# Kernel optimization log

Hardware: AMD Instinct MI355X
Metric: run time of the kernel (lower is better)

Reference implementation:

```python
import jax, jax.numpy as jnp
import numpy as np

B, S, D, H = 4, 1024, 1024, 16
DEPTH = D // H


def setup_inputs() -> dict:
    key = jax.random.key(0)
    ks = jax.random.split(key, 12)
    scale = 1.0 / np.sqrt(D)
    return {
        "query": jax.random.normal(ks[0], (B, S, D), jnp.float32),
        "key_in": jax.random.normal(ks[1], (B, S, D), jnp.float32),
        "value": jax.random.normal(ks[2], (B, S, D), jnp.float32),
        "mask": jnp.zeros((B, 1, 1, S), jnp.float32),
        "wq": jax.random.normal(ks[3], (D, D), jnp.float32) * scale,
        "bq": jnp.zeros((D,), jnp.float32),
        "wk": jax.random.normal(ks[4], (D, D), jnp.float32) * scale,
        "bk": jnp.zeros((D,), jnp.float32),
        "wv": jax.random.normal(ks[5], (D, D), jnp.float32) * scale,
        "bv": jnp.zeros((D,), jnp.float32),
        "wo": jax.random.normal(ks[6], (D, D), jnp.float32) * scale,
        "bo": jnp.zeros((D,), jnp.float32),
    }


def _split_heads(x):
    b, s, _ = x.shape
    return x.reshape(b, s, H, DEPTH).transpose(0, 2, 1, 3)  # [B,H,S,depth]


def reference(query, key_in, value, mask, wq, bq, wk, bk, wv, bv, wo, bo):
    q = _split_heads(query @ wq + bq)
    k = _split_heads(key_in @ wk + bk)
    v = _split_heads(value @ wv + bv)
    # scaled dot-product attention, full O(S^2) scores as in the original
    scores = jnp.einsum("bhqd,bhkd->bhqk", q, k) / jnp.sqrt(jnp.float32(DEPTH))
    scores = scores + mask * (-1e9)
    attn = jax.nn.softmax(scores, axis=-1)
    ctx = jnp.einsum("bhqk,bhkd->bhqd", attn, v)
    concat = ctx.transpose(0, 2, 1, 3).reshape(query.shape[0], -1, D)
    return concat @ wo + bo
```

## Files before the change

kernel.cpp:

```cpp
#include <hip/hip_runtime.h>
#include <hip/hip_bf16.h>
#include <stdint.h>

#define B_ 4
#define S_ 1024
#define D_ 1024
#define H_ 16
#define DEPTH_ 64

typedef __attribute__((ext_vector_type(8))) short bf16x8;
typedef __attribute__((ext_vector_type(4))) float f32x4;
typedef unsigned short ubf16;

#define BAR() do { asm volatile("" ::: "memory"); __builtin_amdgcn_s_barrier(); asm volatile("" ::: "memory"); } while (0)

__device__ __forceinline__ ubf16 f2bf(float f) {
  union { float f; unsigned u; } v; v.f = f;
  unsigned r = v.u + 0x7fffu + ((v.u >> 16) & 1u);
  return (ubf16)(r >> 16);
}

__device__ __forceinline__ void async16(void* lds, const void* g) {
  __builtin_amdgcn_global_load_lds(
      (const __attribute__((address_space(1))) void*)g,
      (__attribute__((address_space(3))) void*)lds, 16, 0, 0);
}

struct Tp4 { const float* W[4]; ubf16* WT[4]; };
__global__ __launch_bounds__(256) void transpose4_bf16(Tp4 a) {
  __shared__ float tile[32][33];
  const float* W = a.W[blockIdx.z];
  ubf16* WT = a.WT[blockIdx.z];
  int n0 = blockIdx.x * 32, k0 = blockIdx.y * 32;
  int tx = threadIdx.x & 31, ty = threadIdx.x >> 5;
#pragma unroll
  for (int i = 0; i < 4; ++i)
    tile[ty + i * 8][tx] = W[(size_t)(k0 + ty + i * 8) * D_ + n0 + tx];
  __syncthreads();
#pragma unroll
  for (int i = 0; i < 4; ++i)
    WT[(size_t)(n0 + ty + i * 8) * D_ + k0 + tx] = f2bf(tile[tx][ty + i * 8]);
}

struct GemmUnitF {
  const float* A; const ubf16* BT; const float* bias; void* out; int mode;
};
struct GemmArgsF { GemmUnitF u[3]; };

__global__ __launch_bounds__(512) void gemm_qkv_fused(GemmArgsF args) {
  const int lin = blockIdx.x;
  const int wg = (lin & 7) * 48 + (lin >> 3);
  const int z = wg >> 7, rr = wg & 127;
  const GemmUnitF gu = args.u[z];
  const int bm0 = (rr >> 2) * 128;
  const int bn0 = (rr & 3) * 256;
  const int tid = threadIdx.x, wid = tid >> 6, lane = tid & 63;
  const int wm = wid >> 2, wn = wid & 3;
  const int l15 = lane & 15, l4 = lane >> 4;
  const int K = 1024;

  __shared__ __align__(16) ubf16 As[2][128 * 32];
  __shared__ __align__(16) ubf16 Bs[2][256 * 32];
  f32x4 acc[4][4] = {};

  const float* aP0;
  {
    int r0 = tid >> 2, s0 = tid & 3, g0 = s0 ^ ((r0 >> 1) & 3);
    aP0 = gu.A + (size_t)(bm0 + r0) * K + g0 * 8;
  }
  const ubf16* bP0; const ubf16* bP1;
  {
    int c0 = tid;        int r0 = c0 >> 2, s0 = c0 & 3, g0 = s0 ^ ((r0 >> 1) & 3);
    int c1 = 512 + tid;  int r1 = c1 >> 2, s1 = c1 & 3, g1 = s1 ^ ((r1 >> 1) & 3);
    bP0 = gu.BT + (size_t)(bn0 + r0) * K + g0 * 8;
    bP1 = gu.BT + (size_t)(bn0 + r1) * K + g1 * 8;
  }
  int aOff[4], bOff[4];
#pragma unroll
  for (int f = 0; f < 4; ++f) {
    int ra = wm * 64 + f * 16 + l15;
    aOff[f] = ra * 64 + (l4 ^ ((ra >> 1) & 3)) * 16;
    int rb = wn * 64 + f * 16 + l15;
    bOff[f] = rb * 64 + (l4 ^ ((rb >> 1) & 3)) * 16;
  }

  {
    f32x4 a00 = *(const f32x4*)aP0, a01 = *(const f32x4*)(aP0 + 4); aP0 += 32;
    async16((char*)&Bs[0][0] + wid * 1024, bP0); bP0 += 32;
    async16((char*)&Bs[0][0] + 8192 + wid * 1024, bP1); bP1 += 32;
    bf16x8 w0;
#pragma unroll
    for (int q = 0; q < 4; ++q) {
      w0[q] = (short)f2bf(a00[q]); w0[4 + q] = (short)f2bf(a01[q]);
    }
    *(bf16x8*)((char*)&As[0][0] + tid * 16) = w0;
    asm volatile("s_waitcnt lgkmcnt(0)" ::: "memory");
  }

#pragma unroll 1
  for (int t = 0; t < 31; ++t) {
    const int cur = t & 1;
    f32x4 a00 = *(const f32x4*)aP0, a01 = *(const f32x4*)(aP0 + 4); aP0 += 32;
    async16((char*)&Bs[cur ^ 1][0] + wid * 1024, bP0); bP0 += 32;
    async16((char*)&Bs[cur ^ 1][0] + 8192 + wid * 1024, bP1); bP1 += 32;
    __builtin_amdgcn_sched_barrier(0);
    asm volatile("s_waitcnt vmcnt(4)" ::: "memory");
    __builtin_amdgcn_s_barrier();
    __builtin_amdgcn_sched_barrier(0);
    bf16x8 af[4], bfr[4];
#pragma unroll
    for (int mi = 0; mi < 4; ++mi)
      af[mi] = *(const bf16x8*)((const char*)&As[cur][0] + aOff[mi]);
#pragma unroll
    for (int ni = 0; ni < 4; ++ni)
      bfr[ni] = *(const bf16x8*)((const char*)&Bs[cur][0] + bOff[ni]);
#pragma unroll
    for (int mi = 0; mi < 4; ++mi)
#pragma unroll
      for (int ni = 0; ni < 4; ++ni)
        acc[mi][ni] = __builtin_amdgcn_mfma_f32_16x16x32_bf16(af[mi], bfr[ni], acc[mi][ni], 0, 0, 0);
    __builtin_amdgcn_sched_barrier(0);
    bf16x8 w0;
#pragma unroll
    for (int q = 0; q < 4; ++q) {
      w0[q] = (short)f2bf(a00[q]); w0[4 + q] = (short)f2bf(a01[q]);
    }
    *(bf16x8*)((char*)&As[cur ^ 1][0] + tid * 16) = w0;
    asm volatile("s_waitcnt lgkmcnt(0)" ::: "memory");
    __builtin_amdgcn_s_barrier();
  }
  asm volatile("s_waitcnt vmcnt(0)" ::: "memory");
  __builtin_amdgcn_s_barrier();
  {
    bf16x8 af[4], bfr[4];
#pragma unroll
    for (int mi = 0; mi < 4; ++mi)
      af[mi] = *(const bf16x8*)((const char*)&As[1][0] + aOff[mi]);
#pragma unroll
    for (int ni = 0; ni < 4; ++ni)
      bfr[ni] = *(const bf16x8*)((const char*)&Bs[1][0] + bOff[ni]);
#pragma unroll
    for (int mi = 0; mi < 4; ++mi)
#pragma unroll
      for (int ni = 0; ni < 4; ++ni)
        acc[mi][ni] = __builtin_amdgcn_mfma_f32_16x16x32_bf16(af[mi], bfr[ni], acc[mi][ni], 0, 0, 0);
  }

  float bv[4];
#pragma unroll
  for (int ni = 0; ni < 4; ++ni) bv[ni] = gu.bias[bn0 + wn * 64 + ni * 16 + l15];
#pragma unroll
  for (int mi = 0; mi < 4; ++mi) {
#pragma unroll
    for (int ni = 0; ni < 4; ++ni) {
#pragma unroll
      for (int r = 0; r < 4; ++r) {
        int m = bm0 + wm * 64 + mi * 16 + l4 * 4 + r;
        int n = bn0 + wn * 64 + ni * 16 + l15;
        float v = acc[mi][ni][r] + bv[ni];
        if (gu.mode == 0) {
          ((ubf16*)gu.out)[(size_t)m * 1024 + n] = f2bf(v);
        } else {
          int b = m >> 10, s = m & 1023, h = n >> 6, d = n & 63;
          ((ubf16*)gu.out)[(((size_t)(b * H_ + h)) * DEPTH_ + d) * S_ + s] = f2bf(v);
        }
      }
    }
  }
}

struct GemmUnit {
  const ubf16* A; const ubf16* BT; const float* bias; void* out; int mode;
};
struct GemmArgs { GemmUnit u[3]; };

__global__ __launch_bounds__(256) void gemm_bt(GemmArgs args, int M, int N) {
  const GemmUnit gu = args.u[blockIdx.z];
  const int orig = blockIdx.x + (blockIdx.y << 3);
  const int xcd = orig & 7, j = orig >> 3;
  const int bm0 = (xcd * 4 + (j & 3)) * 128;
  const int bn0 = (j >> 2) * 128;
  const int tid = threadIdx.x, wid = tid >> 6, lane = tid & 63;
  const int wr = wid >> 1, wc = wid & 1;
  const int l15 = lane & 15, l4 = lane >> 4;
  const int K = 1024;

  __shared__ __align__(16) ubf16 As[2][128 * 32];
  __shared__ __align__(16) ubf16 Bs[2][128 * 32];
  f32x4 acc[4][4] = {};

  const ubf16* aCur[2]; const ubf16* bCur[2];
#pragma unroll
  for (int i = 0; i < 2; ++i) {
    int c = i * 256 + tid;
    int r = c >> 2, s = c & 3;
    int cg = s ^ ((r >> 1) & 3);
    aCur[i] = gu.A + (size_t)(bm0 + r) * K + cg * 8;
    bCur[i] = gu.BT + (size_t)(bn0 + r) * K + cg * 8;
  }
  auto stageAdv = [&](int bf) {
#pragma unroll
    for (int i = 0; i < 2; ++i) {
      async16((char*)&As[bf][0] + i * 4096 + wid * 1024, aCur[i]);
      async16((char*)&Bs[bf][0] + i * 4096 + wid * 1024, bCur[i]);
      aCur[i] += 32; bCur[i] += 32;
    }
  };
  int aOff[4], bOff[4];
#pragma unroll
  for (int f = 0; f < 4; ++f) {
    int ra = wr * 64 + f * 16 + l15;
    aOff[f] = ra * 64 + (l4 ^ ((ra >> 1) & 3)) * 16;
    int rb = wc * 64 + f * 16 + l15;
    bOff[f] = rb * 64 + (l4 ^ ((rb >> 1) & 3)) * 16;
  }

  stageAdv(0);
  for (int t = 0; t < 32; ++t) {
    const int cur = t & 1;
    if (t < 31) {
      stageAdv(cur ^ 1);
      asm volatile("s_waitcnt vmcnt(4)" ::: "memory");
    } else {
      asm volatile("s_waitcnt vmcnt(0)" ::: "memory");
    }
    BAR();
    bf16x8 af[4], bfr[4];
#pragma unroll
    for (int mi = 0; mi < 4; ++mi)
      af[mi] = *(const bf16x8*)((const char*)&As[cur][0] + aOff[mi]);
#pragma unroll
    for (int ni = 0; ni < 4; ++ni)
      bfr[ni] = *(const bf16x8*)((const char*)&Bs[cur][0] + bOff[ni]);
#pragma unroll
    for (int mi = 0; mi < 4; ++mi)
#pragma unroll
      for (int ni = 0; ni < 4; ++ni)
        acc[mi][ni] = __builtin_amdgcn_mfma_f32_16x16x32_bf16(af[mi], bfr[ni], acc[mi][ni], 0, 0, 0);
    BAR();
  }

  float bv[4];
#pragma unroll
  for (int ni = 0; ni < 4; ++ni) bv[ni] = gu.bias[bn0 + wc * 64 + ni * 16 + l15];
#pragma unroll
  for (int mi = 0; mi < 4; ++mi) {
#pragma unroll
    for (int ni = 0; ni < 4; ++ni) {
#pragma unroll
      for (int r = 0; r < 4; ++r) {
        int m = bm0 + wr * 64 + mi * 16 + l4 * 4 + r;
        int n = bn0 + wc * 64 + ni * 16 + l15;
        float v = acc[mi][ni][r] + bv[ni];
        if (gu.mode == 0) {
          ((ubf16*)gu.out)[(size_t)m * N + n] = f2bf(v);
        } else if (gu.mode == 1) {
          int b = m >> 10, s = m & 1023, h = n >> 6, d = n & 63;
          ((ubf16*)gu.out)[(((size_t)(b * H_ + h)) * DEPTH_ + d) * S_ + s] = f2bf(v);
        } else {
          ((float*)gu.out)[(size_t)m * N + n] = v;
        }
      }
    }
  }
}

__global__ __launch_bounds__(512) void attention_fwd(
    const ubf16* __restrict__ Q, const ubf16* __restrict__ Kg,
    const ubf16* __restrict__ VT, const float* __restrict__ mask,
    ubf16* __restrict__ ctx) {
  const int lid = blockIdx.y * 4 + blockIdx.x;
  const int t0 = (lid & 7) * 32 + (lid >> 3);
  const int qt = t0 & 3, bh = t0 >> 2;
  const int b = bh >> 4, h = bh & 15;
  const int tid = threadIdx.x, wid = tid >> 6, lane = tid & 63;
  const int l15 = lane & 15, l4 = lane >> 4;
  const int q0 = qt * 256 + wid * 32;

  __shared__ __align__(16) ubf16 Ks[2][4096];
  __shared__ __align__(16) ubf16 Vs[2][4096];
  __shared__ __align__(16) ubf16 Ps[8][32][72];

  const ubf16* kb = Kg + ((size_t)(b * S_)) * D_ + h * DEPTH_;
  const ubf16* vb = VT + ((size_t)bh) * DEPTH_ * S_;

  bf16x8 aq[2][2];
#pragma unroll
  for (int mi = 0; mi < 2; ++mi)
#pragma unroll
    for (int kk = 0; kk < 2; ++kk)
      aq[mi][kk] = *(const bf16x8*)&Q[((size_t)(b * S_ + q0 + mi * 16 + l15)) * D_ +
                                      h * DEPTH_ + kk * 32 + l4 * 8];

  bf16x8 ones;
#pragma unroll
  for (int j = 0; j < 8; ++j) ones[j] = (short)0x3F80;

  f32x4 cacc[2][4] = {};
  f32x4 csum[2] = {};

  const float* mrow = mask + b * S_;
  const float C1 = 0.125f * 1.44269504f;
  const float CM = -1.0e9f * 1.44269504f;

  auto stage = [&](int bf, int kt) {
    int r = tid >> 3, cg = (tid & 7) ^ (r & 7);
    async16((char*)&Ks[bf][0] + wid * 1024, kb + (size_t)(kt + r) * D_ + cg * 8);
    async16((char*)&Vs[bf][0] + wid * 1024, vb + (size_t)r * S_ + kt + cg * 8);
  };

  stage(0, 0);
  __syncthreads();

  for (int t = 0; t < 16; ++t) {
    const int cur = t & 1;
    const int kt = t * 64;
    if (t < 15) stage(cur ^ 1, kt + 64);

    bf16x8 kf[4][2];
#pragma unroll
    for (int nf = 0; nf < 4; ++nf)
#pragma unroll
      for (int kk = 0; kk < 2; ++kk) {
        int kr = nf * 16 + l15;
        int c16 = (kk * 4 + l4) ^ (kr & 7);
        kf[nf][kk] = *(const bf16x8*)((const char*)&Ks[cur][0] + kr * 128 + c16 * 16);
      }
    bf16x8 vf[4][2];
#pragma unroll
    for (int df = 0; df < 4; ++df)
#pragma unroll
      for (int kk = 0; kk < 2; ++kk) {
        int dr = df * 16 + l15;
        int c16 = (kk * 4 + l4) ^ (dr & 7);
        vf[df][kk] = *(const bf16x8*)((const char*)&Vs[cur][0] + dr * 128 + c16 * 16);
      }

    f32x4 sc[2][4];
#pragma unroll
    for (int mi = 0; mi < 2; ++mi)
#pragma unroll
      for (int nf = 0; nf < 4; ++nf) {
        f32x4 z = {0.f, 0.f, 0.f, 0.f};
        z = __builtin_amdgcn_mfma_f32_16x16x32_bf16(aq[mi][0], kf[nf][0], z, 0, 0, 0);
        z = __builtin_amdgcn_mfma_f32_16x16x32_bf16(aq[mi][1], kf[nf][1], z, 0, 0, 0);
        sc[mi][nf] = z;
      }

    float mvl[4];
#pragma unroll
    for (int nf = 0; nf < 4; ++nf) mvl[nf] = mrow[kt + nf * 16 + l15] * CM;

#pragma unroll
    for (int mi = 0; mi < 2; ++mi)
#pragma unroll
      for (int nf = 0; nf < 4; ++nf)
#pragma unroll
        for (int r = 0; r < 4; ++r) {
          float p = __builtin_amdgcn_exp2f(fmaf(sc[mi][nf][r], C1, mvl[nf]));
          Ps[wid][mi * 16 + l4 * 4 + r][nf * 16 + l15] = f2bf(p);
        }

    bf16x8 pf[2][2];
#pragma unroll
    for (int mi = 0; mi < 2; ++mi)
#pragma unroll
      for (int kk = 0; kk < 2; ++kk)
        pf[mi][kk] = *(const bf16x8*)&Ps[wid][mi * 16 + l15][kk * 32 + l4 * 8];

#pragma unroll
    for (int mi = 0; mi < 2; ++mi) {
#pragma unroll
      for (int df = 0; df < 4; ++df) {
        cacc[mi][df] = __builtin_amdgcn_mfma_f32_16x16x32_bf16(pf[mi][0], vf[df][0], cacc[mi][df], 0, 0, 0);
        cacc[mi][df] = __builtin_amdgcn_mfma_f32_16x16x32_bf16(pf[mi][1], vf[df][1], cacc[mi][df], 0, 0, 0);
      }
      csum[mi] = __builtin_amdgcn_mfma_f32_16x16x32_bf16(pf[mi][0], ones, csum[mi], 0, 0, 0);
      csum[mi] = __builtin_amdgcn_mfma_f32_16x16x32_bf16(pf[mi][1], ones, csum[mi], 0, 0, 0);
    }

    __syncthreads();
  }

#pragma unroll
  for (int mi = 0; mi < 2; ++mi) {
    float inv[4];
#pragma unroll
    for (int r = 0; r < 4; ++r) inv[r] = 1.0f / csum[mi][r];
#pragma unroll
    for (int df = 0; df < 4; ++df)
#pragma unroll
      for (int r = 0; r < 4; ++r) {
        int srow = q0 + mi * 16 + l4 * 4 + r;
        float v = cacc[mi][df][r] * inv[r];
        ctx[((size_t)(b * S_ + srow)) * D_ + h * DEPTH_ + df * 16 + l15] = f2bf(v);
      }
  }
}

extern "C" void kernel_launch(void* const* d_in, const int* in_sizes, int n_in,
                              void* d_out, int out_size, void* d_ws, size_t ws_size,
                              hipStream_t stream) {
  const float* query  = (const float*)d_in[0];
  const float* key_in = (const float*)d_in[1];
  const float* value  = (const float*)d_in[2];
  const float* mask   = (const float*)d_in[3];
  const float* wq = (const float*)d_in[4];
  const float* bq = (const float*)d_in[5];
  const float* wk = (const float*)d_in[6];
  const float* bk = (const float*)d_in[7];
  const float* wv = (const float*)d_in[8];
  const float* bv = (const float*)d_in[9];
  const float* wo = (const float*)d_in[10];
  const float* bo = (const float*)d_in[11];

  char* ws = (char*)d_ws;
  const size_t MB = 1024 * 1024;
  ubf16* WqT = (ubf16*)(ws + 24 * MB);
  ubf16* WkT = (ubf16*)(ws + 26 * MB);
  ubf16* WvT = (ubf16*)(ws + 28 * MB);
  ubf16* WoT = (ubf16*)(ws + 30 * MB);
  ubf16* Qb  = (ubf16*)(ws + 32 * MB);
  ubf16* Kb  = (ubf16*)(ws + 40 * MB);
  ubf16* VTb = (ubf16*)(ws + 48 * MB);
  ubf16* Ctx = (ubf16*)(ws + 56 * MB);

  Tp4 t4;
  t4.W[0] = wq; t4.WT[0] = WqT;
  t4.W[1] = wk; t4.WT[1] = WkT;
  t4.W[2] = wv; t4.WT[2] = WvT;
  t4.W[3] = wo; t4.WT[3] = WoT;
  transpose4_bf16<<<dim3(32, 32, 4), dim3(256), 0, stream>>>(t4);

  GemmArgsF g1;
  g1.u[0] = {query,  WqT, bq, (void*)Qb, 0};
  g1.u[1] = {key_in, WkT, bk, (void*)Kb, 0};
  g1.u[2] = {value,  WvT, bv, (void*)VTb, 1};
  gemm_qkv_fused<<<dim3(384), dim3(512), 0, stream>>>(g1);

  attention_fwd<<<dim3(4, 64), dim3(512), 0, stream>>>(Qb, Kb, VTb, mask, Ctx);

  GemmArgs g2;
  g2.u[0] = {Ctx, WoT, bo, d_out, 2};
  g2.u[1] = g2.u[0];
  g2.u[2] = g2.u[0];
  gemm_bt<<<dim3(8, 32, 1), dim3(256), 0, stream>>>(g2, 4096, 1024);
}
```

Measured before the change: 135.7 us.

## Shrink QKV GEMM tiles to 128x128 and run output GEMM with 8 waves

The fused QKV projection GEMM moves from 128x256 tiles (384 blocks, custom XCD swizzle) to 128x128 tiles on a 3D grid of 768 blocks, with each wave computing 64x32. The output-projection GEMM goes from 256 to 512 threads per block over the same 128x128 tile, so each wave owns a smaller 64x32 sub-tile. Wait counts and staging loads are adjusted to match, and a barrier is added after the QKV prologue. The aim is more blocks and more waves per CU to hide latency, at the cost of less data reuse per tile and more global traffic for the shared operand.

```diff
diff --git a/kernel.cpp b/kernel.cpp
--- a/kernel.cpp
+++ b/kernel.cpp
@@ -48,46 +48,41 @@
 struct GemmArgsF { GemmUnitF u[3]; };
 
 __global__ __launch_bounds__(512) void gemm_qkv_fused(GemmArgsF args) {
-  const int lin = blockIdx.x;
-  const int wg = (lin & 7) * 48 + (lin >> 3);
-  const int z = wg >> 7, rr = wg & 127;
-  const GemmUnitF gu = args.u[z];
-  const int bm0 = (rr >> 2) * 128;
-  const int bn0 = (rr & 3) * 256;
+  const GemmUnitF gu = args.u[blockIdx.z];
+  const int orig = blockIdx.x + (blockIdx.y << 3);
+  const int xcd = orig & 7, j = orig >> 3;
+  const int bm0 = (xcd * 4 + (j & 3)) * 128;
+  const int bn0 = (j >> 2) * 128;
   const int tid = threadIdx.x, wid = tid >> 6, lane = tid & 63;
   const int wm = wid >> 2, wn = wid & 3;
   const int l15 = lane & 15, l4 = lane >> 4;
   const int K = 1024;
 
   __shared__ __align__(16) ubf16 As[2][128 * 32];
-  __shared__ __align__(16) ubf16 Bs[2][256 * 32];
-  f32x4 acc[4][4] = {};
-
-  const float* aP0;
+  __shared__ __align__(16) ubf16 Bs[2][128 * 32];
+  f32x4 acc[4][2] = {};
+
+  const float* aP0; const ubf16* bP0;
   {
     int r0 = tid >> 2, s0 = tid & 3, g0 = s0 ^ ((r0 >> 1) & 3);
     aP0 = gu.A + (size_t)(bm0 + r0) * K + g0 * 8;
-  }
-  const ubf16* bP0; const ubf16* bP1;
-  {
-    int c0 = tid;        int r0 = c0 >> 2, s0 = c0 & 3, g0 = s0 ^ ((r0 >> 1) & 3);
-    int c1 = 512 + tid;  int r1 = c1 >> 2, s1 = c1 & 3, g1 = s1 ^ ((r1 >> 1) & 3);
     bP0 = gu.BT + (size_t)(bn0 + r0) * K + g0 * 8;
-    bP1 = gu.BT + (size_t)(bn0 + r1) * K + g1 * 8;
-  }
-  int aOff[4], bOff[4];
+  }
+  int aOff[4], bOff[2];
 #pragma unroll
   for (int f = 0; f < 4; ++f) {
     int ra = wm * 64 + f * 16 + l15;
     aOff[f] = ra * 64 + (l4 ^ ((ra >> 1) & 3)) * 16;
-    int rb = wn * 64 + f * 16 + l15;
+  }
+#pragma unroll
+  for (int f = 0; f < 2; ++f) {
+    int rb = wn * 32 + f * 16 + l15;
     bOff[f] = rb * 64 + (l4 ^ ((rb >> 1) & 3)) * 16;
   }
 
   {
     f32x4 a00 = *(const f32x4*)aP0, a01 = *(const f32x4*)(aP0 + 4); aP0 += 32;
     async16((char*)&Bs[0][0] + wid * 1024, bP0); bP0 += 32;
-    async16((char*)&Bs[0][0] + 8192 + wid * 1024, bP1); bP1 += 32;
     bf16x8 w0;
 #pragma unroll
     for (int q = 0; q < 4; ++q) {
@@ -95,6 +90,7 @@
     }
     *(bf16x8*)((char*)&As[0][0] + tid * 16) = w0;
     asm volatile("s_waitcnt lgkmcnt(0)" ::: "memory");
+    BAR();
   }
 
 #pragma unroll 1
@@ -102,22 +98,21 @@
     const int cur = t & 1;
     f32x4 a00 = *(const f32x4*)aP0, a01 = *(const f32x4*)(aP0 + 4); aP0 += 32;
     async16((char*)&Bs[cur ^ 1][0] + wid * 1024, bP0); bP0 += 32;
-    async16((char*)&Bs[cur ^ 1][0] + 8192 + wid * 1024, bP1); bP1 += 32;
     __builtin_amdgcn_sched_barrier(0);
-    asm volatile("s_waitcnt vmcnt(4)" ::: "memory");
+    asm volatile("s_waitcnt vmcnt(3)" ::: "memory");
     __builtin_amdgcn_s_barrier();
     __builtin_amdgcn_sched_barrier(0);
-    bf16x8 af[4], bfr[4];
+    bf16x8 af[4], bfr[2];
 #pragma unroll
     for (int mi = 0; mi < 4; ++mi)
       af[mi] = *(const bf16x8*)((const char*)&As[cur][0] + aOff[mi]);
 #pragma unroll
-    for (int ni = 0; ni < 4; ++ni)
+    for (int ni = 0; ni < 2; ++ni)
       bfr[ni] = *(const bf16x8*)((const char*)&Bs[cur][0] + bOff[ni]);
 #pragma unroll
     for (int mi = 0; mi < 4; ++mi)
 #pragma unroll
-      for (int ni = 0; ni < 4; ++ni)
+      for (int ni = 0; ni < 2; ++ni)
         acc[mi][ni] = __builtin_amdgcn_mfma_f32_16x16x32_bf16(af[mi], bfr[ni], acc[mi][ni], 0, 0, 0);
     __builtin_amdgcn_sched_barrier(0);
     bf16x8 w0;
@@ -132,31 +127,31 @@
   asm volatile("s_waitcnt vmcnt(0)" ::: "memory");
   __builtin_amdgcn_s_barrier();
   {
-    bf16x8 af[4], bfr[4];
+    bf16x8 af[4], bfr[2];
 #pragma unroll
     for (int mi = 0; mi < 4; ++mi)
       af[mi] = *(const bf16x8*)((const char*)&As[1][0] + aOff[mi]);
 #pragma unroll
-    for (int ni = 0; ni < 4; ++ni)
+    for (int ni = 0; ni < 2; ++ni)
       bfr[ni] = *(const bf16x8*)((const char*)&Bs[1][0] + bOff[ni]);
 #pragma unroll
     for (int mi = 0; mi < 4; ++mi)
 #pragma unroll
-      for (int ni = 0; ni < 4; ++ni)
+      for (int ni = 0; ni < 2; ++ni)
         acc[mi][ni] = __builtin_amdgcn_mfma_f32_16x16x32_bf16(af[mi], bfr[ni], acc[mi][ni], 0, 0, 0);
   }
 
-  float bv[4];
-#pragma unroll
-  for (int ni = 0; ni < 4; ++ni) bv[ni] = gu.bias[bn0 + wn * 64 + ni * 16 + l15];
+  float bv[2];
+#pragma unroll
+  for (int ni = 0; ni < 2; ++ni) bv[ni] = gu.bias[bn0 + wn * 32 + ni * 16 + l15];
 #pragma unroll
   for (int mi = 0; mi < 4; ++mi) {
 #pragma unroll
-    for (int ni = 0; ni < 4; ++ni) {
+    for (int ni = 0; ni < 2; ++ni) {
 #pragma unroll
       for (int r = 0; r < 4; ++r) {
         int m = bm0 + wm * 64 + mi * 16 + l4 * 4 + r;
-        int n = bn0 + wn * 64 + ni * 16 + l15;
+        int n = bn0 + wn * 32 + ni * 16 + l15;
         float v = acc[mi][ni][r] + bv[ni];
         if (gu.mode == 0) {
           ((ubf16*)gu.out)[(size_t)m * 1024 + n] = f2bf(v);
@@ -174,44 +169,41 @@
 };
 struct GemmArgs { GemmUnit u[3]; };
 
-__global__ __launch_bounds__(256) void gemm_bt(GemmArgs args, int M, int N) {
+__global__ __launch_bounds__(512) void gemm_bt(GemmArgs args, int M, int N) {
   const GemmUnit gu = args.u[blockIdx.z];
   const int orig = blockIdx.x + (blockIdx.y << 3);
   const int xcd = orig & 7, j = orig >> 3;
   const int bm0 = (xcd * 4 + (j & 3)) * 128;
   const int bn0 = (j >> 2) * 128;
   const int tid = threadIdx.x, wid = tid >> 6, lane = tid & 63;
-  const int wr = wid >> 1, wc = wid & 1;
+  const int wm = wid >> 2, wn = wid & 3;
   const int l15 = lane & 15, l4 = lane >> 4;
   const int K = 1024;
 
   __shared__ __align__(16) ubf16 As[2][128 * 32];
   __shared__ __align__(16) ubf16 Bs[2][128 * 32];
-  f32x4 acc[4][4] = {};
-
-  const ubf16* aCur[2]; const ubf16* bCur[2];
-#pragma unroll
-  for (int i = 0; i < 2; ++i) {
-    int c = i * 256 + tid;
-    int r = c >> 2, s = c & 3;
+  f32x4 acc[4][2] = {};
+
+  const ubf16* aCur; const ubf16* bCur;
+  {
+    int r = tid >> 2, s = tid & 3;
     int cg = s ^ ((r >> 1) & 3);
-    aCur[i] = gu.A + (size_t)(bm0 + r) * K + cg * 8;
-    bCur[i] = gu.BT + (size_t)(bn0 + r) * K + cg * 8;
+    aCur = gu.A + (size_t)(bm0 + r) * K + cg * 8;
+    bCur = gu.BT + (size_t)(bn0 + r) * K + cg * 8;
   }
   auto stageAdv = [&](int bf) {
-#pragma unroll
-    for (int i = 0; i < 2; ++i) {
-      async16((char*)&As[bf][0] + i * 4096 + wid * 1024, aCur[i]);
-      async16((char*)&Bs[bf][0] + i * 4096 + wid * 1024, bCur[i]);
-      aCur[i] += 32; bCur[i] += 32;
-    }
+    async16((char*)&As[bf][0] + wid * 1024, aCur); aCur += 32;
+    async16((char*)&Bs[bf][0] + wid * 1024, bCur); bCur += 32;
   };
-  int aOff[4], bOff[4];
+  int aOff[4], bOff[2];
 #pragma unroll
   for (int f = 0; f < 4; ++f) {
-    int ra = wr * 64 + f * 16 + l15;
+    int ra = wm * 64 + f * 16 + l15;
     aOff[f] = ra * 64 + (l4 ^ ((ra >> 1) & 3)) * 16;
-    int rb = wc * 64 + f * 16 + l15;
+  }
+#pragma unroll
+  for (int f = 0; f < 2; ++f) {
+    int rb = wn * 32 + f * 16 + l15;
     bOff[f] = rb * 64 + (l4 ^ ((rb >> 1) & 3)) * 16;
   }
 
@@ -220,37 +212,37 @@
     const int cur = t & 1;
     if (t < 31) {
       stageAdv(cur ^ 1);
-      asm volatile("s_waitcnt vmcnt(4)" ::: "memory");
+      asm volatile("s_waitcnt vmcnt(2)" ::: "memory");
     } else {
       asm volatile("s_waitcnt vmcnt(0)" ::: "memory");
     }
     BAR();
-    bf16x8 af[4], bfr[4];
+    bf16x8 af[4], bfr[2];
 #pragma unroll
     for (int mi = 0; mi < 4; ++mi)
       af[mi] = *(const bf16x8*)((const char*)&As[cur][0] + aOff[mi]);
 #pragma unroll
-    for (int ni = 0; ni < 4; ++ni)
+    for (int ni = 0; ni < 2; ++ni)
       bfr[ni] = *(const bf16x8*)((const char*)&Bs[cur][0] + bOff[ni]);
 #pragma unroll
     for (int mi = 0; mi < 4; ++mi)
 #pragma unroll
-      for (int ni = 0; ni < 4; ++ni)
+      for (int ni = 0; ni < 2; ++ni)
         acc[mi][ni] = __builtin_amdgcn_mfma_f32_16x16x32_bf16(af[mi], bfr[ni], acc[mi][ni], 0, 0, 0);
     BAR();
   }
 
-  float bv[4];
-#pragma unroll
-  for (int ni = 0; ni < 4; ++ni) bv[ni] = gu.bias[bn0 + wc * 64 + ni * 16 + l15];
+  float bv[2];
+#pragma unroll
+  for (int ni = 0; ni < 2; ++ni) bv[ni] = gu.bias[bn0 + wn * 32 + ni * 16 + l15];
 #pragma unroll
   for (int mi = 0; mi < 4; ++mi) {
 #pragma unroll
-    for (int ni = 0; ni < 4; ++ni) {
+    for (int ni = 0; ni < 2; ++ni) {
 #pragma unroll
       for (int r = 0; r < 4; ++r) {
-        int m = bm0 + wr * 64 + mi * 16 + l4 * 4 + r;
-        int n = bn0 + wc * 64 + ni * 16 + l15;
+        int m = bm0 + wm * 64 + mi * 16 + l4 * 4 + r;
+        int n = bn0 + wn * 32 + ni * 16 + l15;
         float v = acc[mi][ni][r] + bv[ni];
         if (gu.mode == 0) {
           ((ubf16*)gu.out)[(size_t)m * N + n] = f2bf(v);
@@ -436,7 +428,7 @@
   g1.u[0] = {query,  WqT, bq, (void*)Qb, 0};
   g1.u[1] = {key_in, WkT, bk, (void*)Kb, 0};
   g1.u[2] = {value,  WvT, bv, (void*)VTb, 1};
-  gemm_qkv_fused<<<dim3(384), dim3(512), 0, stream>>>(g1);
+  gemm_qkv_fused<<<dim3(8, 32, 3), dim3(512), 0, stream>>>(g1);
 
   attention_fwd<<<dim3(4, 64), dim3(512), 0, stream>>>(Qb, Kb, VTb, mask, Ctx);
 
@@ -444,5 +436,5 @@
   g2.u[0] = {Ctx, WoT, bo, d_out, 2};
   g2.u[1] = g2.u[0];
   g2.u[2] = g2.u[0];
-  gemm_bt<<<dim3(8, 32, 1), dim3(256), 0, stream>>>(g2, 4096, 1024);
-}
+  gemm_bt<<<dim3(8, 32, 1), dim3(512), 0, stream>>>(g2, 4096, 1024);
+}
```

New measurement: 109.7 us, median of 2. 19.1% less time.
